# Optimization experiments

Hardware: AMD Instinct MI355X
Metric: run time of the kernel (lower is better)

## Reference

```python
import jax, jax.numpy as jnp
import numpy as np

B, T, N, E = 4, 16, 1024, 16384
F_IN, H, FF, NH, L, C = 128, 256, 1024, 8, 2, 10
HD = H // NH
EPS = 1e-5


def setup_inputs() -> dict:
    key = jax.random.key(0)
    ks = jax.random.split(key, 12)
    g = lambda k, s: jax.random.normal(k, s, dtype=jnp.float32) * 0.02
    return {
        "x": jax.random.normal(ks[0], (B, T, N, F_IN), dtype=jnp.float32),
        "edge_index": jax.random.randint(ks[1], (B, T, 2, E), 0, N, dtype=jnp.int32),
        # GraphSAGE layer 1 (PyG SAGEConv: lin_l on mean-aggregated neighbors, lin_r on self)
        "sage1_Wl": g(ks[2], (F_IN, H)), "sage1_bl": jnp.zeros((H,), jnp.float32),
        "sage1_Wr": g(ks[3], (F_IN, H)),
        # GraphSAGE layer 2
        "sage2_Wl": g(ks[4], (H, H)), "sage2_bl": jnp.zeros((H,), jnp.float32),
        "sage2_Wr": g(ks[5], (H, H)),
        # TransformerEncoder, stacked over L layers
        "Wqkv": g(ks[6], (L, H, 3 * H)), "bqkv": jnp.zeros((L, 3 * H), jnp.float32),
        "Wo": g(ks[7], (L, H, H)), "bo": jnp.zeros((L, H), jnp.float32),
        "ln1_s": jnp.ones((L, H), jnp.float32), "ln1_b": jnp.zeros((L, H), jnp.float32),
        "W1": g(ks[8], (L, H, FF)), "b1": jnp.zeros((L, FF), jnp.float32),
        "W2": g(ks[9], (L, FF, H)), "b2": jnp.zeros((L, H), jnp.float32),
        "ln2_s": jnp.ones((L, H), jnp.float32), "ln2_b": jnp.zeros((L, H), jnp.float32),
        # final classifier
        "fc_W": g(ks[10], (H, C)), "fc_b": jnp.zeros((C,), jnp.float32),
    }


def _sage_conv(x, src, dst, Wl, bl, Wr):
    # mean neighbor aggregation: for each target node, mean of source features
    deg = jax.ops.segment_sum(jnp.ones((E,), x.dtype), dst, num_segments=N)
    agg = jax.ops.segment_sum(x[src], dst, num_segments=N)  # [N, F]
    agg = agg / jnp.clip(deg, 1.0)[:, None]
    return agg @ Wl + bl + x @ Wr


def _layernorm(x, s, b):
    m = jnp.mean(x, axis=-1, keepdims=True)
    v = jnp.var(x, axis=-1, keepdims=True)
    return (x - m) * jax.lax.rsqrt(v + EPS) * s + b


def _encoder_layer(h, Wqkv, bqkv, Wo, bo, ln1_s, ln1_b, W1, b1, W2, b2, ln2_s, ln2_b):
    # h: [B, T, H] -- post-norm (PyTorch default norm_first=False), relu FFN
    qkv = h @ Wqkv + bqkv  # [B, T, 3H]
    q, k, v = jnp.split(qkv, 3, axis=-1)
    sp = lambda t: t.reshape(B, T, NH, HD).transpose(0, 2, 1, 3)  # [B, NH, T, HD]
    q, k, v = sp(q), sp(k), sp(v)
    scores = jnp.einsum("bhqd,bhkd->bhqk", q, k) / np.sqrt(HD).astype(np.float32)
    attn = jax.nn.softmax(scores, axis=-1)
    ctx = jnp.einsum("bhqk,bhkd->bhqd", attn, v)
    ctx = ctx.transpose(0, 2, 1, 3).reshape(B, T, H)
    h = _layernorm(h + ctx @ Wo + bo, ln1_s, ln1_b)
    ffn = jax.nn.relu(h @ W1 + b1) @ W2 + b2
    return _layernorm(h + ffn, ln2_s, ln2_b)


def reference(x, edge_index, sage1_Wl, sage1_bl, sage1_Wr, sage2_Wl, sage2_bl,
              sage2_Wr, Wqkv, bqkv, Wo, bo, ln1_s, ln1_b, W1, b1, W2, b2,
              ln2_s, ln2_b, fc_W, fc_b):
    xf = x.reshape(B * T, N, F_IN)
    ef = edge_index.reshape(B * T, 2, E)

    def per_graph(xg, eg):
        src, dst = eg[0], eg[1]
        h = jax.nn.relu(_sage_conv(xg, src, dst, sage1_Wl, sage1_bl, sage1_Wr))
        h = _sage_conv(h, src, dst, sage2_Wl, sage2_bl, sage2_Wr)
        return jnp.mean(h, axis=0)  # mean-pool over nodes -> [H]

    emb = jax.vmap(per_graph)(xf, ef).reshape(B, T, H)

    h = emb
    for l in range(L):
        h = _encoder_layer(h, Wqkv[l], bqkv[l], Wo[l], bo[l], ln1_s[l], ln1_b[l],
                           W1[l], b1[l], W2[l], b2[l], ln2_s[l], ln2_b[l])
    return h[:, -1, :] @ fc_W + fc_b  # [B, C]
```

## Files before the change

### kernel.cpp

```cpp
#include <hip/hip_runtime.h>
#include <hip/hip_bf16.h>

#define Bc 4
#define Tc 16
#define Nc 1024
#define Ec 16384
#define FIN 128
#define Hc 256
#define FFc 1024
#define NHc 8
#define Lc 2
#define HDc 32
#define Gc 64
#define EPSc 1e-5f

typedef __bf16 v8bf __attribute__((ext_vector_type(8)));
typedef float v4f __attribute__((ext_vector_type(4)));

__global__ void pack_w_kernel(const float* __restrict__ Wl, const float* __restrict__ Wr,
                              __bf16* __restrict__ pH, __bf16* __restrict__ pL) {
    int bid = blockIdx.x;
    int t = threadIdx.x;
    int lane = t >> 3, j = t & 7;
    int kc = bid >> 4, nt = bid & 15;
    int k = kc * 32 + ((lane >> 4) << 3) + j;
    int n = nt * 16 + (lane & 15);
    float w = (k < 128) ? Wl[(size_t)k * Hc + n] : Wr[(size_t)(k - 128) * Hc + n];
    __bf16 hi = (__bf16)w;
    __bf16 lo = (__bf16)(w - (float)hi);
    pH[bid * 512 + t] = hi;
    pL[bid * 512 + t] = lo;
}

__global__ __launch_bounds__(1024) void csr_kernel(
        const int* __restrict__ ei, float* __restrict__ invdeg, float* __restrict__ cw,
        int* __restrict__ off, unsigned short* __restrict__ elist, float* __restrict__ uv) {
    __shared__ int degs[Nc];
    __shared__ float inv[Nc];
    __shared__ float cl[Nc];
    __shared__ int wsum[16];
    int g = blockIdx.x, t = threadIdx.x;
    const int* src = ei + (size_t)g * 2 * Ec;
    const int* dst = src + Ec;
    if (t < 512) uv[g * 512 + t] = 0.f;
    degs[t] = 0; cl[t] = 0.f;
    __syncthreads();
    for (int e = t; e < Ec; e += 1024) atomicAdd(&degs[dst[e] & (Nc - 1)], 1);
    __syncthreads();
    float iv = 1.0f / fmaxf((float)degs[t], 1.0f);
    inv[t] = iv;
    invdeg[g * Nc + t] = iv;
    __syncthreads();
    for (int e = t; e < Ec; e += 1024) atomicAdd(&cl[src[e] & (Nc - 1)], inv[dst[e] & (Nc - 1)]);
    __syncthreads();
    cw[g * Nc + t] = cl[t];
    int own = degs[t];
    int lane = t & 63, wv = t >> 6;
    int val = own;
#pragma unroll
    for (int ofs = 1; ofs < 64; ofs <<= 1) {
        int v = __shfl_up(val, ofs, 64);
        if (lane >= ofs) val += v;
    }
    if (lane == 63) wsum[wv] = val;
    __syncthreads();
    if (wv == 0 && lane < 16) {
        int wval = wsum[lane];
#pragma unroll
        for (int ofs = 1; ofs < 16; ofs <<= 1) {
            int v = __shfl_up(wval, ofs, 64);
            if (lane >= ofs) wval += v;
        }
        wsum[lane] = wval;
    }
    __syncthreads();
    int incl = val + ((wv > 0) ? wsum[wv - 1] : 0);
    int excl = incl - own;
    off[g * 1032 + t] = excl;
    if (t == 1023) off[g * 1032 + Nc] = incl;
    degs[t] = excl;
    __syncthreads();
    for (int e = t; e < Ec; e += 1024) {
        int d = dst[e] & (Nc - 1);
        int slot = atomicAdd(&degs[d], 1);
        elist[(size_t)g * Ec + slot] = (unsigned short)(src[e] & (Nc - 1));
    }
}

__global__ __launch_bounds__(512) void sage_kernel(
        const float* __restrict__ x, const unsigned short* __restrict__ elist,
        const int* __restrict__ off, const float* __restrict__ invdeg,
        const float* __restrict__ cw, const __bf16* __restrict__ pH,
        const __bf16* __restrict__ pL, const float* __restrict__ bias,
        float* __restrict__ uv) {
    __shared__ float aggL[32 * 132];
    __shared__ float xL[32 * 132];
    __shared__ float lu[256], lv[256];
    int tid = threadIdx.x;
    int bid = blockIdx.x;
    int g = bid & 63, cc = bid >> 6, r0 = cc * 32;
    const unsigned short* el = elist + (size_t)g * Ec;
    const float* xg = x + (size_t)g * Nc * FIN;
    if (tid < 256) { lu[tid] = 0.f; lv[tid] = 0.f; }

    {
        int lr = tid >> 4, ch = tid & 15;
        int n = r0 + lr;
        int o0 = off[g * 1032 + n], o1 = off[g * 1032 + n + 1];
        float4 a0 = make_float4(0.f, 0.f, 0.f, 0.f);
        float4 a1 = make_float4(0.f, 0.f, 0.f, 0.f);
        const float* xc = xg + ch * 8;
        int e = o0;
        for (; e + 8 <= o1; e += 8) {
            int s[8];
#pragma unroll
            for (int j = 0; j < 8; ++j) s[j] = el[e + j];
            float4 v0[8], v1[8];
#pragma unroll
            for (int j = 0; j < 8; ++j) {
                const float4* xp = (const float4*)(xc + (size_t)s[j] * FIN);
                v0[j] = xp[0]; v1[j] = xp[1];
            }
#pragma unroll
            for (int j = 0; j < 8; ++j) {
                a0.x += v0[j].x; a0.y += v0[j].y; a0.z += v0[j].z; a0.w += v0[j].w;
                a1.x += v1[j].x; a1.y += v1[j].y; a1.z += v1[j].z; a1.w += v1[j].w;
            }
        }
        for (; e < o1; ++e) {
            const float4* xp = (const float4*)(xc + (size_t)el[e] * FIN);
            float4 v0 = xp[0], v1 = xp[1];
            a0.x += v0.x; a0.y += v0.y; a0.z += v0.z; a0.w += v0.w;
            a1.x += v1.x; a1.y += v1.y; a1.z += v1.z; a1.w += v1.w;
        }
        float iv = invdeg[g * Nc + n];
        float* dp = &aggL[lr * 132 + ch * 8];
        dp[0] = a0.x * iv; dp[1] = a0.y * iv; dp[2] = a0.z * iv; dp[3] = a0.w * iv;
        dp[4] = a1.x * iv; dp[5] = a1.y * iv; dp[6] = a1.z * iv; dp[7] = a1.w * iv;
    }
    for (int i = tid; i < 1024; i += 512) {
        int lr = i >> 5, kq = i & 31;
        *(float4*)&xL[lr * 132 + kq * 4] = *(const float4*)&xg[(size_t)(r0 + lr) * FIN + kq * 4];
    }
    __syncthreads();

    int w = tid >> 6, lane = tid & 63, quad = lane >> 4;
    int mt = w & 1, nh = w >> 1;
    int lrow = mt * 16 + (lane & 15);
    v4f acc[4];
#pragma unroll
    for (int i = 0; i < 4; ++i) acc[i] = (v4f)0.f;
    for (int kc = 0; kc < 8; ++kc) {
        const float* ap = (kc < 4) ? &aggL[lrow * 132 + kc * 32 + quad * 8]
                                   : &xL[lrow * 132 + (kc - 4) * 32 + quad * 8];
        float4 f0 = *(const float4*)ap;
        float4 f1 = *(const float4*)(ap + 4);
        float av[8] = {f0.x, f0.y, f0.z, f0.w, f1.x, f1.y, f1.z, f1.w};
        v8bf aH, aL;
#pragma unroll
        for (int j = 0; j < 8; ++j) {
            __bf16 hb = (__bf16)av[j];
            aH[j] = hb;
            aL[j] = (__bf16)(av[j] - (float)hb);
        }
#pragma unroll
        for (int i = 0; i < 4; ++i) {
            int nt = nh * 4 + i;
            v8bf bH = *(const v8bf*)(pH + ((size_t)(kc * 16 + nt) * 64 + lane) * 8);
            v8bf bL = *(const v8bf*)(pL + ((size_t)(kc * 16 + nt) * 64 + lane) * 8);
            acc[i] = __builtin_amdgcn_mfma_f32_16x16x32_bf16(aH, bH, acc[i], 0, 0, 0);
            acc[i] = __builtin_amdgcn_mfma_f32_16x16x32_bf16(aL, bH, acc[i], 0, 0, 0);
            acc[i] = __builtin_amdgcn_mfma_f32_16x16x32_bf16(aH, bL, acc[i], 0, 0, 0);
        }
    }

    float c4[4];
    int nb = g * Nc + r0 + mt * 16 + quad * 4;
#pragma unroll
    for (int r = 0; r < 4; ++r) c4[r] = cw[nb + r];
#pragma unroll
    for (int i = 0; i < 4; ++i) {
        int col = (nh * 4 + i) * 16 + (lane & 15);
        float bcol = bias[col];
        float su = 0.f, sv = 0.f;
#pragma unroll
        for (int r = 0; r < 4; ++r) {
            float val = fmaxf(acc[i][r] + bcol, 0.f);
            sv += val;
            su += c4[r] * val;
        }
        su += __shfl_xor(su, 16); sv += __shfl_xor(sv, 16);
        su += __shfl_xor(su, 32); sv += __shfl_xor(sv, 32);
        if (quad == 0) { atomicAdd(&lu[col], su); atomicAdd(&lv[col], sv); }
    }
    __syncthreads();
    if (tid < 256) {
        atomicAdd(&uv[g * 512 + tid], lu[tid]);
        atomicAdd(&uv[g * 512 + 256 + tid], lv[tid]);
    }
}

__global__ __launch_bounds__(512) void emb_kernel(
        const float* __restrict__ uv, const float* __restrict__ Wl2,
        const float* __restrict__ bl2, const float* __restrict__ Wr2,
        float* __restrict__ h) {
    __shared__ float s[512];
    __shared__ float r2[512];
    int g = blockIdx.x, tid = threadIdx.x;
    s[tid] = uv[g * 512 + tid] * (1.0f / Nc);
    __syncthreads();
    int col = tid & 255, p = tid >> 8;
    float val = 0.f;
    if (p == 0) { for (int k = 0; k < 256; ++k) val += s[k] * Wl2[(size_t)k * Hc + col]; }
    else        { for (int k = 0; k < 256; ++k) val += s[256 + k] * Wr2[(size_t)k * Hc + col]; }
    r2[tid] = val;
    __syncthreads();
    if (tid < 256) h[g * Hc + tid] = bl2[tid] + r2[tid] + r2[tid + 256];
}

__global__ __launch_bounds__(1024) void layer_kernel(
        const float* __restrict__ hin, float* __restrict__ hout,
        const float* __restrict__ Wqkv, const float* __restrict__ bqkv,
        const float* __restrict__ Wo, const float* __restrict__ bo,
        const float* __restrict__ s1, const float* __restrict__ b1ln,
        const float* __restrict__ W1, const float* __restrict__ bf1,
        const float* __restrict__ W2, const float* __restrict__ bf2,
        const float* __restrict__ s2, const float* __restrict__ b2ln,
        const float* __restrict__ fcW, const float* __restrict__ fcb,
        float* __restrict__ out, int l, int last) {
    __shared__ float hT[256 * 16];
    __shared__ float kvL[16 * 512];
    __shared__ float q[256];
    __shared__ float sc[8][17];
    __shared__ float ctx[256];
    __shared__ float r2[512];
    __shared__ float red[256];
    __shared__ float rF[2048];
    __shared__ float fLs[1024];
    __shared__ float h1L[256];
    int t = blockIdx.x, tid = threadIdx.x;
    int b = t >> 4, own = t & 15;
    for (int i = tid; i < 4096; i += 1024) {
        int j = i >> 8, k = i & 255;
        hT[k * 16 + j] = hin[(size_t)(b * 16 + j) * 256 + k];
    }
    __syncthreads();
    {
        int col = tid & 511, jh = tid >> 9;
        const float* W = Wqkv + (size_t)l * Hc * 768 + 256 + col;
        float acc[8], s0[8];
#pragma unroll
        for (int j = 0; j < 8; ++j) acc[j] = 0.f;
        for (int k = 0; k < 128; ++k) {
            float w = W[(size_t)k * 768];
            const float4* hk = (const float4*)&hT[k * 16 + jh * 8];
            float4 h0 = hk[0], h1 = hk[1];
            acc[0] += h0.x * w; acc[1] += h0.y * w; acc[2] += h0.z * w; acc[3] += h0.w * w;
            acc[4] += h1.x * w; acc[5] += h1.y * w; acc[6] += h1.z * w; acc[7] += h1.w * w;
        }
#pragma unroll
        for (int j = 0; j < 8; ++j) { s0[j] = acc[j]; acc[j] = 0.f; }
        for (int k = 128; k < 256; ++k) {
            float w = W[(size_t)k * 768];
            const float4* hk = (const float4*)&hT[k * 16 + jh * 8];
            float4 h0 = hk[0], h1 = hk[1];
            acc[0] += h0.x * w; acc[1] += h0.y * w; acc[2] += h0.z * w; acc[3] += h0.w * w;
            acc[4] += h1.x * w; acc[5] += h1.y * w; acc[6] += h1.z * w; acc[7] += h1.w * w;
        }
        float bq = bqkv[(size_t)l * 768 + 256 + col];
#pragma unroll
        for (int j = 0; j < 8; ++j) kvL[(size_t)(jh * 8 + j) * 512 + col] = bq + s0[j] + acc[j];
    }
    if (tid < 256) {
        const float* W = Wqkv + (size_t)l * Hc * 768 + tid;
        float p0 = 0.f, p1 = 0.f;
        for (int k = 0; k < 128; ++k) p0 += hT[k * 16 + own] * W[(size_t)k * 768];
        for (int k = 128; k < 256; ++k) p1 += hT[k * 16 + own] * W[(size_t)k * 768];
        q[tid] = bqkv[(size_t)l * 768 + tid] + p0 + p1;
    }
    __syncthreads();
    if (tid < 128) {
        int hd = tid >> 4, jj = tid & 15;
        float s = 0.f;
#pragma unroll
        for (int d = 0; d < 32; ++d) s += q[hd * 32 + d] * kvL[jj * 512 + hd * 32 + d];
        sc[hd][jj] = s * 0.17677669529663687f;
    }
    __syncthreads();
    if (tid < 8) {
        float m = sc[tid][0];
        for (int j = 1; j < 16; ++j) m = fmaxf(m, sc[tid][j]);
        float e[16], sum = 0.f;
        for (int j = 0; j < 16; ++j) { e[j] = expf(sc[tid][j] - m); sum += e[j]; }
        float inv = 1.0f / sum;
        for (int j = 0; j < 16; ++j) sc[tid][j] = e[j] * inv;
    }
    __syncthreads();
    if (tid < 256) {
        int hd = tid >> 5, d = tid & 31;
        float o = 0.f;
#pragma unroll
        for (int j = 0; j < 16; ++j) o += sc[hd][j] * kvL[j * 512 + 256 + hd * 32 + d];
        ctx[tid] = o;
    }
    __syncthreads();
    if (tid < 512) {
        int col = tid & 255, half = tid >> 8;
        const float* W = Wo + (size_t)l * 65536;
        float pv = 0.f;
        int k0 = half * 128;
        for (int k = 0; k < 128; ++k) pv += ctx[k0 + k] * W[(size_t)(k0 + k) * 256 + col];
        r2[tid] = pv;
    }
    __syncthreads();
    float val = 0.f;
    if (tid < 256) {
        val = hT[tid * 16 + own] + bo[(size_t)l * 256 + tid] + r2[tid] + r2[tid + 256];
        red[tid] = val;
    }
    __syncthreads();
    for (int s = 128; s > 0; s >>= 1) { if (tid < s) red[tid] += red[tid + s]; __syncthreads(); }
    float m1 = red[0] * (1.0f / 256.0f);
    __syncthreads();
    float d1 = val - m1;
    if (tid < 256) red[tid] = d1 * d1;
    __syncthreads();
    for (int s = 128; s > 0; s >>= 1) { if (tid < s) red[tid] += red[tid + s]; __syncthreads(); }
    float v1 = red[0] * (1.0f / 256.0f);
    if (tid < 256)
        h1L[tid] = d1 * rsqrtf(v1 + EPSc) * s1[(size_t)l * 256 + tid] + b1ln[(size_t)l * 256 + tid];
    __syncthreads();
#pragma unroll
    for (int pass = 0; pass < 2; ++pass) {
        int pid = pass * 1024 + tid;
        int cg = pid >> 9, ch = pid & 511;
        int col = cg * 256 + (ch & 255), half = ch >> 8;
        const float* W = W1 + (size_t)l * 262144;
        float v = 0.f;
        int k0 = half * 128;
        for (int k = 0; k < 128; ++k) v += h1L[k0 + k] * W[(size_t)(k0 + k) * 1024 + col];
        rF[pid] = v;
    }
    __syncthreads();
    {
        int cg = tid >> 8, c8 = tid & 255;
        fLs[tid] = fmaxf(bf1[(size_t)l * 1024 + tid] + rF[cg * 512 + c8] + rF[cg * 512 + 256 + c8], 0.f);
    }
    __syncthreads();
    {
        int col = tid & 255, kq = tid >> 8;
        const float* W = W2 + (size_t)l * 262144;
        float p = 0.f;
        int k0 = kq * 256;
        for (int k = 0; k < 256; ++k) p += fLs[k0 + k] * W[(size_t)(k0 + k) * 256 + col];
        rF[tid] = p;
    }
    __syncthreads();
    float val2 = 0.f;
    if (tid < 256) {
        val2 = h1L[tid] + bf2[(size_t)l * 256 + tid]
             + rF[tid] + rF[tid + 256] + rF[tid + 512] + rF[tid + 768];
        red[tid] = val2;
    }
    __syncthreads();
    for (int s = 128; s > 0; s >>= 1) { if (tid < s) red[tid] += red[tid + s]; __syncthreads(); }
    float m2 = red[0] * (1.0f / 256.0f);
    __syncthreads();
    float d2 = (tid < 256) ? (val2 - m2) : 0.f;
    if (tid < 256) red[tid] = d2 * d2;
    __syncthreads();
    for (int s = 128; s > 0; s >>= 1) { if (tid < s) red[tid] += red[tid + s]; __syncthreads(); }
    float var2 = red[0] * (1.0f / 256.0f);
    float hn = 0.f;
    if (tid < 256) {
        hn = d2 * rsqrtf(var2 + EPSc) * s2[(size_t)l * 256 + tid] + b2ln[(size_t)l * 256 + tid];
        hout[(size_t)t * 256 + tid] = hn;
    }
    if (last && own == 15) {
        __syncthreads();
        if (tid < 256) red[tid] = hn;
        __syncthreads();
        if (tid < 10) {
            float fv = fcb[tid];
            for (int k = 0; k < 256; ++k) fv += red[k] * fcW[(size_t)k * 10 + tid];
            out[b * 10 + tid] = fv;
        }
    }
}

extern "C" void kernel_launch(void* const* d_in, const int* in_sizes, int n_in,
                              void* d_out, int out_size, void* d_ws, size_t ws_size,
                              hipStream_t stream) {
    (void)in_sizes; (void)n_in; (void)out_size; (void)ws_size;
    const float* x    = (const float*)d_in[0];
    const int*   ei   = (const int*)d_in[1];
    const float* s1Wl = (const float*)d_in[2];
    const float* s1bl = (const float*)d_in[3];
    const float* s1Wr = (const float*)d_in[4];
    const float* s2Wl = (const float*)d_in[5];
    const float* s2bl = (const float*)d_in[6];
    const float* s2Wr = (const float*)d_in[7];
    const float* Wqkv = (const float*)d_in[8];
    const float* bqkv = (const float*)d_in[9];
    const float* Wo   = (const float*)d_in[10];
    const float* bo   = (const float*)d_in[11];
    const float* ln1s = (const float*)d_in[12];
    const float* ln1b = (const float*)d_in[13];
    const float* W1   = (const float*)d_in[14];
    const float* b1   = (const float*)d_in[15];
    const float* W2   = (const float*)d_in[16];
    const float* b2   = (const float*)d_in[17];
    const float* ln2s = (const float*)d_in[18];
    const float* ln2b = (const float*)d_in[19];
    const float* fcW  = (const float*)d_in[20];
    const float* fcb  = (const float*)d_in[21];

    char* ws = (char*)d_ws;
    __bf16*         packWH = (__bf16*)(ws + 0);
    __bf16*         packWL = (__bf16*)(ws + 131072);
    float*          invdeg = (float*)(ws + 262144);
    float*          cw     = (float*)(ws + 524288);
    int*            off    = (int*)(ws + 786432);
    unsigned short* elist  = (unsigned short*)(ws + 1050624);
    float*          uv     = (float*)(ws + 3147776);
    float*          h      = (float*)(ws + 3278848);
    float*          h2     = (float*)(ws + 3344384);

    pack_w_kernel<<<128, 512, 0, stream>>>(s1Wl, s1Wr, packWH, packWL);
    csr_kernel<<<Gc, 1024, 0, stream>>>(ei, invdeg, cw, off, elist, uv);
    sage_kernel<<<Gc * 32, 512, 0, stream>>>(x, elist, off, invdeg, cw, packWH, packWL, s1bl, uv);
    emb_kernel<<<Gc, 512, 0, stream>>>(uv, s2Wl, s2bl, s2Wr, h);
    layer_kernel<<<Gc, 1024, 0, stream>>>(h, h2, Wqkv, bqkv, Wo, bo, ln1s, ln1b,
                                          W1, b1, W2, b2, ln2s, ln2b, fcW, fcb,
                                          (float*)d_out, 0, 0);
    layer_kernel<<<Gc, 1024, 0, stream>>>(h2, h, Wqkv, bqkv, Wo, bo, ln1s, ln1b,
                                          W1, b1, W2, b2, ln2s, ln2b, fcW, fcb,
                                          (float*)d_out, 1, 1);
}
```

Baseline: 346.0 us.

## Split QKV projection into separate kernel to remove redundant per-block K/V compute

Each layer's QKV projection moves into its own kernel that computes every token's q, k and v once, using 192 blocks, and writes them to a workspace buffer. The attention/FFN kernel then reads K/V for its batch from global memory into padded shared memory. Before, each of the 64 blocks recomputed K and V for all 16 tokens of its batch. This removes that 16x redundant work and spreads the projection over more blocks, at the cost of two extra kernel launches and a global round trip for qkv.

```diff
diff --git a/kernel.cpp b/kernel.cpp
--- a/kernel.cpp
+++ b/kernel.cpp
@@ -218,9 +218,31 @@
     if (tid < 256) h[g * Hc + tid] = bl2[tid] + r2[tid] + r2[tid + 256];
 }
 
-__global__ __launch_bounds__(1024) void layer_kernel(
+__global__ __launch_bounds__(512) void qkv_kernel(
+        const float* __restrict__ h, const float* __restrict__ Wqkv,
+        const float* __restrict__ bqkv, float* __restrict__ qkv, int l) {
+    __shared__ float hr[256];
+    __shared__ float r2[512];
+    int bid = blockIdx.x;
+    int gi = bid / 3, seg = bid % 3;
+    int tid = threadIdx.x;
+    if (tid < 256) hr[tid] = h[gi * Hc + tid];
+    __syncthreads();
+    int col = seg * 256 + (tid & 255);
+    int half = tid >> 8;
+    const float* W = Wqkv + (size_t)l * Hc * 768;
+    float val = 0.f;
+    int k0 = half * 128;
+    for (int k = 0; k < 128; ++k) val += hr[k0 + k] * W[(size_t)(k0 + k) * 768 + col];
+    r2[tid] = val;
+    __syncthreads();
+    if (tid < 256) qkv[gi * 768 + col] = bqkv[(size_t)l * 768 + col] + r2[tid] + r2[tid + 256];
+}
+
+#define KVS 516
+__global__ __launch_bounds__(1024) void rest_kernel(
         const float* __restrict__ hin, float* __restrict__ hout,
-        const float* __restrict__ Wqkv, const float* __restrict__ bqkv,
+        const float* __restrict__ qkvg,
         const float* __restrict__ Wo, const float* __restrict__ bo,
         const float* __restrict__ s1, const float* __restrict__ b1ln,
         const float* __restrict__ W1, const float* __restrict__ bf1,
@@ -228,8 +250,7 @@
         const float* __restrict__ s2, const float* __restrict__ b2ln,
         const float* __restrict__ fcW, const float* __restrict__ fcb,
         float* __restrict__ out, int l, int last) {
-    __shared__ float hT[256 * 16];
-    __shared__ float kvL[16 * 512];
+    __shared__ float kv[16 * KVS];
     __shared__ float q[256];
     __shared__ float sc[8][17];
     __shared__ float ctx[256];
@@ -239,51 +260,19 @@
     __shared__ float fLs[1024];
     __shared__ float h1L[256];
     int t = blockIdx.x, tid = threadIdx.x;
-    int b = t >> 4, own = t & 15;
-    for (int i = tid; i < 4096; i += 1024) {
-        int j = i >> 8, k = i & 255;
-        hT[k * 16 + j] = hin[(size_t)(b * 16 + j) * 256 + k];
-    }
-    __syncthreads();
-    {
-        int col = tid & 511, jh = tid >> 9;
-        const float* W = Wqkv + (size_t)l * Hc * 768 + 256 + col;
-        float acc[8], s0[8];
-#pragma unroll
-        for (int j = 0; j < 8; ++j) acc[j] = 0.f;
-        for (int k = 0; k < 128; ++k) {
-            float w = W[(size_t)k * 768];
-            const float4* hk = (const float4*)&hT[k * 16 + jh * 8];
-            float4 h0 = hk[0], h1 = hk[1];
-            acc[0] += h0.x * w; acc[1] += h0.y * w; acc[2] += h0.z * w; acc[3] += h0.w * w;
-            acc[4] += h1.x * w; acc[5] += h1.y * w; acc[6] += h1.z * w; acc[7] += h1.w * w;
-        }
-#pragma unroll
-        for (int j = 0; j < 8; ++j) { s0[j] = acc[j]; acc[j] = 0.f; }
-        for (int k = 128; k < 256; ++k) {
-            float w = W[(size_t)k * 768];
-            const float4* hk = (const float4*)&hT[k * 16 + jh * 8];
-            float4 h0 = hk[0], h1 = hk[1];
-            acc[0] += h0.x * w; acc[1] += h0.y * w; acc[2] += h0.z * w; acc[3] += h0.w * w;
-            acc[4] += h1.x * w; acc[5] += h1.y * w; acc[6] += h1.z * w; acc[7] += h1.w * w;
-        }
-        float bq = bqkv[(size_t)l * 768 + 256 + col];
-#pragma unroll
-        for (int j = 0; j < 8; ++j) kvL[(size_t)(jh * 8 + j) * 512 + col] = bq + s0[j] + acc[j];
-    }
-    if (tid < 256) {
-        const float* W = Wqkv + (size_t)l * Hc * 768 + tid;
-        float p0 = 0.f, p1 = 0.f;
-        for (int k = 0; k < 128; ++k) p0 += hT[k * 16 + own] * W[(size_t)k * 768];
-        for (int k = 128; k < 256; ++k) p1 += hT[k * 16 + own] * W[(size_t)k * 768];
-        q[tid] = bqkv[(size_t)l * 768 + tid] + p0 + p1;
-    }
+    int b = t >> 4;
+    const float* qb = qkvg + (size_t)(b * 16) * 768;
+    for (int i = tid; i < 8192; i += 1024) {
+        int j = i >> 9, d = i & 511;
+        kv[j * KVS + d] = qb[(size_t)j * 768 + 256 + d];
+    }
+    if (tid < 256) q[tid] = qkvg[(size_t)t * 768 + tid];
     __syncthreads();
     if (tid < 128) {
         int hd = tid >> 4, jj = tid & 15;
         float s = 0.f;
 #pragma unroll
-        for (int d = 0; d < 32; ++d) s += q[hd * 32 + d] * kvL[jj * 512 + hd * 32 + d];
+        for (int d = 0; d < 32; ++d) s += q[hd * 32 + d] * kv[jj * KVS + hd * 32 + d];
         sc[hd][jj] = s * 0.17677669529663687f;
     }
     __syncthreads();
@@ -300,7 +289,7 @@
         int hd = tid >> 5, d = tid & 31;
         float o = 0.f;
 #pragma unroll
-        for (int j = 0; j < 16; ++j) o += sc[hd][j] * kvL[j * 512 + 256 + hd * 32 + d];
+        for (int j = 0; j < 16; ++j) o += sc[hd][j] * kv[j * KVS + 256 + hd * 32 + d];
         ctx[tid] = o;
     }
     __syncthreads();
@@ -315,7 +304,7 @@
     __syncthreads();
     float val = 0.f;
     if (tid < 256) {
-        val = hT[tid * 16 + own] + bo[(size_t)l * 256 + tid] + r2[tid] + r2[tid + 256];
+        val = hin[(size_t)t * 256 + tid] + bo[(size_t)l * 256 + tid] + r2[tid] + r2[tid + 256];
         red[tid] = val;
     }
     __syncthreads();
@@ -376,14 +365,15 @@
         hn = d2 * rsqrtf(var2 + EPSc) * s2[(size_t)l * 256 + tid] + b2ln[(size_t)l * 256 + tid];
         hout[(size_t)t * 256 + tid] = hn;
     }
-    if (last && own == 15) {
+    if (last && (t & 15) == 15) {
         __syncthreads();
         if (tid < 256) red[tid] = hn;
         __syncthreads();
         if (tid < 10) {
+            int bb = t >> 4;
             float fv = fcb[tid];
             for (int k = 0; k < 256; ++k) fv += red[k] * fcW[(size_t)k * 10 + tid];
-            out[b * 10 + tid] = fv;
+            out[bb * 10 + tid] = fv;
         }
     }
 }
@@ -425,15 +415,18 @@
     float*          uv     = (float*)(ws + 3147776);
     float*          h      = (float*)(ws + 3278848);
     float*          h2     = (float*)(ws + 3344384);
+    float*          qkvg   = (float*)(ws + 3409920);
 
     pack_w_kernel<<<128, 512, 0, stream>>>(s1Wl, s1Wr, packWH, packWL);
     csr_kernel<<<Gc, 1024, 0, stream>>>(ei, invdeg, cw, off, elist, uv);
     sage_kernel<<<Gc * 32, 512, 0, stream>>>(x, elist, off, invdeg, cw, packWH, packWL, s1bl, uv);
     emb_kernel<<<Gc, 512, 0, stream>>>(uv, s2Wl, s2bl, s2Wr, h);
-    layer_kernel<<<Gc, 1024, 0, stream>>>(h, h2, Wqkv, bqkv, Wo, bo, ln1s, ln1b,
-                                          W1, b1, W2, b2, ln2s, ln2b, fcW, fcb,
-                                          (float*)d_out, 0, 0);
-    layer_kernel<<<Gc, 1024, 0, stream>>>(h2, h, Wqkv, bqkv, Wo, bo, ln1s, ln1b,
-                                          W1, b1, W2, b2, ln2s, ln2b, fcW, fcb,
-                                          (float*)d_out, 1, 1);
-}
+    qkv_kernel<<<Gc * 3, 512, 0, stream>>>(h, Wqkv, bqkv, qkvg, 0);
+    rest_kernel<<<Gc, 1024, 0, stream>>>(h, h2, qkvg, Wo, bo, ln1s, ln1b,
+                                         W1, b1, W2, b2, ln2s, ln2b, fcW, fcb,
+                                         (float*)d_out, 0, 0);
+    qkv_kernel<<<Gc * 3, 512, 0, stream>>>(h2, Wqkv, bqkv, qkvg, 1);
+    rest_kernel<<<Gc, 1024, 0, stream>>>(h2, h, qkvg, Wo, bo, ln1s, ln1b,
+                                         W1, b1, W2, b2, ln2s, ln2b, fcW, fcb,
+                                         (float*)d_out, 1, 1);
+}
```

Result: faster. 317.6 us (-8.2%).
